# Performance work log

Hardware: AMD Instinct MI355X
Metric: run time of the kernel (lower is better)

## Reference

```python
import jax, jax.numpy as jnp
import numpy as np

N_HEADS = 4
D_HEAD = 64
SCALE = D_HEAD ** -0.5


def setup_inputs() -> dict:
    key = jax.random.key(0)
    k0, k1, k2, k3, k4 = jax.random.split(key, 5)
    C = 256
    return {
        "x": jax.random.normal(k0, (32, C, 32, 32), dtype=jnp.float32),
        "W_qkv": jax.random.normal(k1, (C, 3 * N_HEADS * D_HEAD), dtype=jnp.float32) * 0.02,
        "b_qkv": jax.random.normal(k2, (3 * N_HEADS * D_HEAD,), dtype=jnp.float32) * 0.02,
        "W_out": jax.random.normal(k3, (C, C), dtype=jnp.float32) * 0.02,
        "b_out": jax.random.normal(k4, (C,), dtype=jnp.float32) * 0.02,
    }


def reference(x, W_qkv, b_qkv, W_out, b_out):
    b, c, h, w = x.shape
    # [B, C, H, W] -> [B, S, C], S = H*W  (NOTE: GroupNorm is defined in the
    # original module but never applied in forward; we match that exactly.)
    xs = x.reshape(b, c, h * w).transpose(0, 2, 1)
    qkv = (xs @ W_qkv + b_qkv).reshape(b, -1, N_HEADS, 3 * D_HEAD)
    q, k, v = jnp.split(qkv, 3, axis=-1)  # each [B, S, H, D]
    scores = jnp.einsum('bihd,bjhd->bijh', q, k) * SCALE  # [B, S, S, H]
    attn = jax.nn.softmax(scores, axis=2)  # softmax over key index j
    res = jnp.einsum('bijh,bjhd->bihd', attn, v).reshape(b, -1, N_HEADS * D_HEAD)
    res = res @ W_out + b_out + xs
    return res.transpose(0, 2, 1).reshape(b, c, h, w)
```

## Files before the change

### kernel.cpp

```cpp
#include <hip/hip_runtime.h>

#define NH 4
#define DH 64
#define SS 1024
#define CC 256

typedef __attribute__((ext_vector_type(8))) short short8;
typedef __attribute__((ext_vector_type(4))) float floatx4;
typedef __attribute__((ext_vector_type(16))) float floatx16;
typedef __attribute__((ext_vector_type(2))) unsigned uint2v;

#define MFMA16(a, b, c) __builtin_amdgcn_mfma_f32_16x16x32_bf16(a, b, c, 0, 0, 0)
#define MFMA32(a, b, c) __builtin_amdgcn_mfma_f32_32x32x16_bf16(a, b, c, 0, 0, 0)

#define QSCALE 0.18033688011112042f

__device__ __forceinline__ short f2bf(float f) {
    union { float f; unsigned u; } v; v.f = f;
    unsigned r = (v.u + 0x7fffu + ((v.u >> 16) & 1u)) >> 16;
    return (short)r;
}
__device__ __forceinline__ unsigned bfrn(float f) {
    union { float f; unsigned u; } v; v.f = f;
    return (v.u + 0x7fffu + ((v.u >> 16) & 1u)) >> 16;
}
__device__ __forceinline__ unsigned pk2_trunc(float a, float b) {
    union { float f; unsigned u; } ua, ub; ua.f = a; ub.f = b;
    return (ua.u >> 16) | (ub.u & 0xFFFF0000u);
}
__device__ __forceinline__ unsigned pk2_rn(float a, float b) {
    return bfrn(a) | (bfrn(b) << 16);
}

__global__ __launch_bounds__(256) void k_prep(const float* __restrict__ x,
                                              const float* __restrict__ Wqkv,
                                              const float* __restrict__ Wout,
                                              short* __restrict__ xs,
                                              short* __restrict__ Wqkv_t,
                                              short* __restrict__ Wout_t) {
    int bid = blockIdx.x;
    if (bid < 2048) {
        __shared__ float tile[64][65];
        int b = bid >> 6;
        int s0 = ((bid >> 2) & 15) * 64;
        int c0 = (bid & 3) * 64;
        int t = threadIdx.x;
        int tx = t & 63, ty = t >> 6;
        for (int i = 0; i < 16; ++i) {
            int c = ty + i * 4;
            tile[tx][c] = x[((b * CC) + (c0 + c)) * SS + s0 + tx];
        }
        __syncthreads();
        for (int i = 0; i < 8; ++i) {
            int s = (t >> 5) + i * 8;
            int cp = (t & 31) * 2;
            short2 v;
            v.x = f2bf(tile[s][cp]);
            v.y = f2bf(tile[s][cp + 1]);
            *(short2*)(&xs[((b * SS) + (s0 + s)) * CC + c0 + cp]) = v;
        }
    } else {
        int idx = (bid - 2048) * 256 + threadIdx.x;
        if (idx < 768 * 256) {
            int n = idx >> 8, k = idx & 255;
            Wqkv_t[idx] = f2bf(Wqkv[k * 768 + n]);
        } else {
            int j = idx - 768 * 256;
            int c = j >> 8, k = j & 255;
            Wout_t[j] = f2bf(Wout[k * 256 + c]);
        }
    }
}

__global__ __launch_bounds__(256) void k_qkv(const short* __restrict__ xs,
                                             const short* __restrict__ Wt,
                                             const float* __restrict__ bqkv,
                                             short* __restrict__ qtw,
                                             short* __restrict__ kw,
                                             short* __restrict__ vtw) {
    __shared__ short smem[10240];
    short* As = smem;
    short* Bs = smem + 5120;
    int bid = blockIdx.x;
    int idx = bid >> 3;
    int m0 = ((bid & 7) * 32 + idx / 6) * 128;
    int n0 = (idx % 6) * 128;
    int t = threadIdx.x;
    int lane = t & 63, wid = t >> 6;
    int wr = wid >> 1, wc = wid & 1;
    int c16 = lane & 15, qd = lane >> 4;

    floatx4 acc[4][4] = {};
    short8 pa[2], pb[2];

    for (int j = 0; j < 2; ++j) {
        int id = j * 256 + t, row = id >> 2, cc = id & 3;
        pa[j] = *(const short8*)(&xs[(m0 + row) * CC + cc * 8]);
        pb[j] = *(const short8*)(&Wt[(n0 + row) * CC + cc * 8]);
    }
    for (int kt = 0; kt < 8; ++kt) {
        if (kt) __syncthreads();
        for (int j = 0; j < 2; ++j) {
            int id = j * 256 + t, row = id >> 2, cc = id & 3;
            *(short8*)(&As[row * 40 + cc * 8]) = pa[j];
            *(short8*)(&Bs[row * 40 + cc * 8]) = pb[j];
        }
        __syncthreads();
        if (kt < 7) {
            for (int j = 0; j < 2; ++j) {
                int id = j * 256 + t, row = id >> 2, cc = id & 3;
                pa[j] = *(const short8*)(&xs[(m0 + row) * CC + (kt + 1) * 32 + cc * 8]);
                pb[j] = *(const short8*)(&Wt[(n0 + row) * CC + (kt + 1) * 32 + cc * 8]);
            }
        }
        short8 av[4], bv[4];
        for (int i = 0; i < 4; ++i) {
            av[i] = *(const short8*)(&As[(wr * 64 + i * 16 + c16) * 40 + qd * 8]);
            bv[i] = *(const short8*)(&Bs[(wc * 64 + i * 16 + c16) * 40 + qd * 8]);
        }
        for (int mi = 0; mi < 4; ++mi)
            for (int ni = 0; ni < 4; ++ni)
                acc[mi][ni] = MFMA16(av[mi], bv[ni], acc[mi][ni]);
    }

    int b = m0 >> 10, sbase = m0 & 1023;
    int seg = (n0 >> 6) + wc;
    float bias4[4];
    for (int ni = 0; ni < 4; ++ni)
        bias4[ni] = bqkv[n0 + wc * 64 + ni * 16 + c16];

    int seg0 = n0 >> 6;
    short* Tt = smem;
    for (int s2 = 0; s2 < 2; ++s2) {
        int sg = seg0 + s2;
        int type = sg % 3;
        if (type == 1) continue;
        float sc = (type == 0) ? QSCALE : 1.f;
        __syncthreads();
        if (wc == s2) {
            for (int mi = 0; mi < 4; ++mi)
                for (int ni = 0; ni < 4; ++ni)
                    for (int r = 0; r < 4; ++r)
                        Tt[(ni * 16 + c16) * 136 + wr * 64 + mi * 16 + qd * 4 + r] =
                            f2bf((acc[mi][ni][r] + bias4[ni]) * sc);
        }
        __syncthreads();
        short* dst = ((type == 0) ? qtw : vtw) + (size_t)((b * NH + sg / 3) * DH) * SS + sbase;
        for (int it = 0; it < 4; ++it) {
            int c = it * 256 + t;
            int d = c >> 4, off = (c & 15) * 8;
            *(short8*)(dst + (size_t)d * SS + off) =
                *(const short8*)(&Tt[d * 136 + off]);
        }
    }

    int kseg = (seg0 % 3 == 1) ? seg0 : (((seg0 + 1) % 3 == 1) ? seg0 + 1 : -1);
    if (kseg >= 0) {
        short* Kt = smem;
        __syncthreads();
        if (seg == kseg) {
            for (int mi = 0; mi < 4; ++mi)
                for (int ni = 0; ni < 4; ++ni)
                    for (int r = 0; r < 4; ++r)
                        Kt[(wr * 64 + mi * 16 + qd * 4 + r) * 72 + ni * 16 + c16] =
                            f2bf(acc[mi][ni][r] + bias4[ni]);
        }
        __syncthreads();
        int bhk = b * NH + kseg / 3;
        int srow = t >> 1, dh = (t & 1) * 32;
        short* gdst = &kw[(size_t)(bhk * SS + sbase + srow) * DH + dh];
        const short* lsrc = &Kt[srow * 72 + dh];
        for (int k = 0; k < 4; ++k)
            *(short8*)(gdst + k * 8) = *(const short8*)(lsrc + k * 8);
    }
}

__global__ __launch_bounds__(256) void k_attn(const short* __restrict__ qtw,
                                              const short* __restrict__ kw,
                                              const short* __restrict__ vtw,
                                              short* __restrict__ res) {
    __shared__ __align__(16) short Ks[128 * 72];
    __shared__ __align__(16) short Vts[64 * 136];
    int bid = blockIdx.x;
    int q0 = (bid >> 7) * 128;
    int bh = bid & 127;
    int t = threadIdx.x;
    int lane = t & 63, w = t >> 6;
    int l31 = lane & 31, hi = lane >> 5;
    const short* qp = qtw + (size_t)bh * DH * SS;
    const short* kp = kw + (size_t)bh * SS * DH;
    const short* vp = vtw + (size_t)bh * DH * SS;

    short8 qfrag[4];
    {
        int s = q0 + w * 32 + l31;
        for (int kd = 0; kd < 4; ++kd) {
            short8 q;
            for (int e = 0; e < 8; ++e)
                q[e] = qp[(size_t)(kd * 16 + hi * 8 + e) * SS + s];
            qfrag[kd] = q;
        }
    }

    float l_i = 0.f;
    floatx16 o_acc[2] = {};

    short8 kreg[4], vreg[4];
    for (int j = 0; j < 4; ++j) {
        int L = j * 256 + t;
        int kr = L >> 3, kc = (L & 7) * 8;
        kreg[j] = *(const short8*)(&kp[kr * DH + kc]);
        int vd = L >> 4, vc = (L & 15) * 8;
        vreg[j] = *(const short8*)(&vp[vd * SS + vc]);
    }

    for (int kt = 0; kt < 8; ++kt) {
        if (kt) __syncthreads();
        for (int j = 0; j < 4; ++j) {
            int L = j * 256 + t;
            int kr = L >> 3, kc = (L & 7) * 8;
            *(short8*)(&Ks[kr * 72 + kc]) = kreg[j];
            int vd = L >> 4, vc = (L & 15) * 8;
            *(short8*)(&Vts[vd * 136 + vc]) = vreg[j];
        }
        __syncthreads();
        if (kt < 7) {
            for (int j = 0; j < 4; ++j) {
                int L = j * 256 + t;
                int kr = L >> 3, kc = (L & 7) * 8;
                kreg[j] = *(const short8*)(&kp[((kt + 1) * 128 + kr) * DH + kc]);
                int vd = L >> 4, vc = (L & 15) * 8;
                vreg[j] = *(const short8*)(&vp[vd * SS + (kt + 1) * 128 + vc]);
            }
        }

#pragma unroll
        for (int jt = 0; jt < 4; ++jt) {
            short8 kf[4];
#pragma unroll
            for (int kd = 0; kd < 4; ++kd)
                kf[kd] = *(const short8*)(&Ks[(jt * 32 + l31) * 72 + kd * 16 + hi * 8]);
            short8 vf0[2], vf1[2];
#pragma unroll
            for (int dt = 0; dt < 2; ++dt) {
                vf0[dt] = *(const short8*)(&Vts[(dt * 32 + l31) * 136 + (jt * 2 + 0) * 16 + hi * 8]);
                vf1[dt] = *(const short8*)(&Vts[(dt * 32 + l31) * 136 + (jt * 2 + 1) * 16 + hi * 8]);
            }

            floatx16 sacc = {};
            __builtin_amdgcn_s_setprio(1);
#pragma unroll
            for (int kd = 0; kd < 4; ++kd)
                sacc = MFMA32(kf[kd], qfrag[kd], sacc);
            __builtin_amdgcn_s_setprio(0);

            float ls = 0.f;
            unsigned u[8];
#pragma unroll
            for (int r = 0; r < 16; r += 2) {
                float e0 = __builtin_amdgcn_exp2f(sacc[r]);
                float e1 = __builtin_amdgcn_exp2f(sacc[r + 1]);
                ls += e0 + e1;
                u[r >> 1] = pk2_trunc(e0, e1);
            }
            l_i += ls;

            uint2v r02 = __builtin_amdgcn_permlane32_swap(u[0], u[2], false, false);
            uint2v r13 = __builtin_amdgcn_permlane32_swap(u[1], u[3], false, false);
            uint2v r46 = __builtin_amdgcn_permlane32_swap(u[4], u[6], false, false);
            uint2v r57 = __builtin_amdgcn_permlane32_swap(u[5], u[7], false, false);
            union { unsigned w[4]; short8 s; } pf0, pf1;
            pf0.w[0] = r02[0]; pf0.w[1] = r13[0]; pf0.w[2] = r02[1]; pf0.w[3] = r13[1];
            pf1.w[0] = r46[0]; pf1.w[1] = r57[0]; pf1.w[2] = r46[1]; pf1.w[3] = r57[1];

            __builtin_amdgcn_s_setprio(1);
#pragma unroll
            for (int dt = 0; dt < 2; ++dt) {
                o_acc[dt] = MFMA32(vf0[dt], pf0.s, o_acc[dt]);
                o_acc[dt] = MFMA32(vf1[dt], pf1.s, o_acc[dt]);
            }
            __builtin_amdgcn_s_setprio(0);
        }
    }

    int b = bh >> 2, h = bh & 3;
    {
        float l = l_i;
        l += __shfl_xor(l, 32);
        float inv = 1.f / l;
        int s = q0 + w * 32 + l31;
        long base = (long)(b * SS + s) * CC + h * DH;
#pragma unroll
        for (int dt = 0; dt < 2; ++dt) {
#pragma unroll
            for (int q = 0; q < 4; ++q) {
                int d = dt * 32 + q * 8 + hi * 4;
                uint2 ow;
                ow.x = pk2_rn(o_acc[dt][q * 4 + 0] * inv, o_acc[dt][q * 4 + 1] * inv);
                ow.y = pk2_rn(o_acc[dt][q * 4 + 2] * inv, o_acc[dt][q * 4 + 3] * inv);
                *(uint2*)(&res[base + d]) = ow;
            }
        }
    }
}

__global__ __launch_bounds__(256) void k_out(const short* __restrict__ res,
                                             const short* __restrict__ Wot,
                                             const float* __restrict__ bout,
                                             const float* __restrict__ x,
                                             float* __restrict__ out) {
    __shared__ short As[2][64 * 40];
    __shared__ short Bs[2][128 * 40];
    int b = blockIdx.z;
    int m0 = blockIdx.y * 64;
    int n0 = blockIdx.x * 128;
    int t = threadIdx.x;
    int lane = t & 63, wid = t >> 6;
    int wr = wid >> 1, wc = wid & 1;
    int c16 = lane & 15, qd = lane >> 4;

    floatx4 acc[2][4] = {};
    int arow = t >> 2, ac4 = (t & 3) * 8;
    int brow0 = t >> 2, bc0 = (t & 3) * 8;
    int brow1 = brow0 + 64;
    short8 pa, pb0, pb1;
    pa  = *(const short8*)(&Wot[(m0 + arow) * CC + ac4]);
    pb0 = *(const short8*)(&res[(b * SS + n0 + brow0) * CC + bc0]);
    pb1 = *(const short8*)(&res[(b * SS + n0 + brow1) * CC + bc0]);
    *(short8*)(&As[0][arow * 40 + ac4]) = pa;
    *(short8*)(&Bs[0][brow0 * 40 + bc0]) = pb0;
    *(short8*)(&Bs[0][brow1 * 40 + bc0]) = pb1;
    __syncthreads();

    int cur = 0;
    for (int kt = 0; kt < 8; ++kt) {
        if (kt < 7) {
            pa  = *(const short8*)(&Wot[(m0 + arow) * CC + (kt + 1) * 32 + ac4]);
            pb0 = *(const short8*)(&res[(b * SS + n0 + brow0) * CC + (kt + 1) * 32 + bc0]);
            pb1 = *(const short8*)(&res[(b * SS + n0 + brow1) * CC + (kt + 1) * 32 + bc0]);
        }
        short8 av[2], bv[4];
        for (int i = 0; i < 2; ++i)
            av[i] = *(const short8*)(&As[cur][(wr * 32 + i * 16 + c16) * 40 + qd * 8]);
        for (int i = 0; i < 4; ++i)
            bv[i] = *(const short8*)(&Bs[cur][(wc * 64 + i * 16 + c16) * 40 + qd * 8]);
        for (int mi = 0; mi < 2; ++mi)
            for (int ni = 0; ni < 4; ++ni)
                acc[mi][ni] = MFMA16(av[mi], bv[ni], acc[mi][ni]);
        if (kt < 7) {
            *(short8*)(&As[cur ^ 1][arow * 40 + ac4]) = pa;
            *(short8*)(&Bs[cur ^ 1][brow0 * 40 + bc0]) = pb0;
            *(short8*)(&Bs[cur ^ 1][brow1 * 40 + bc0]) = pb1;
            __syncthreads();
            cur ^= 1;
        }
    }

    for (int mi = 0; mi < 2; ++mi) {
        for (int r = 0; r < 4; ++r) {
            int c = m0 + wr * 32 + mi * 16 + qd * 4 + r;
            float bias = bout[c];
            for (int ni = 0; ni < 4; ++ni) {
                int s = n0 + wc * 64 + ni * 16 + c16;
                float v = acc[mi][ni][r] + bias + x[((b * CC) + c) * SS + s];
                out[((b * CC) + c) * SS + s] = v;
            }
        }
    }
}

extern "C" void kernel_launch(void* const* d_in, const int* in_sizes, int n_in,
                              void* d_out, int out_size, void* d_ws, size_t ws_size,
                              hipStream_t stream) {
    const float* x    = (const float*)d_in[0];
    const float* Wqkv = (const float*)d_in[1];
    const float* bqkv = (const float*)d_in[2];
    const float* Wout = (const float*)d_in[3];
    const float* bout = (const float*)d_in[4];
    float* out = (float*)d_out;

    char* ws = (char*)d_ws;
    short* xs_res = (short*)(ws);
    short* qtw    = (short*)(ws + 16777216);
    short* kw     = (short*)(ws + 33554432);
    short* vtw    = (short*)(ws + 50331648);
    short* Wqkv_t = (short*)(ws + 67108864);
    short* Wout_t = (short*)(ws + 67502080);

    k_prep<<<dim3(3072), 256, 0, stream>>>(x, Wqkv, Wout, xs_res, Wqkv_t, Wout_t);
    k_qkv<<<dim3(1536), 256, 0, stream>>>(xs_res, Wqkv_t, bqkv, qtw, kw, vtw);
    k_attn<<<dim3(1024), 256, 0, stream>>>(qtw, kw, vtw, xs_res);
    k_out<<<dim3(8, 4, 32), 256, 0, stream>>>(xs_res, Wout_t, bout, x, out);
}
```

Before: 179.2 us.

## Use 512-thread attention blocks with 256 queries and 64-key tiles

The attention kernel now runs 8 waves per block, covering 256 query rows each, over half as many blocks. K/V tiles shrink from 128 to 64 keys, giving 16 iterations with one register-prefetched short8 per thread. The goal is more K/V reuse per shared-memory load and less LDS use per block. The trade-off is twice as many barriers per key span and fewer blocks to spread across CUs, which could hurt occupancy or load balance.

```diff
diff --git a/kernel.cpp b/kernel.cpp
--- a/kernel.cpp
+++ b/kernel.cpp
@@ -175,14 +175,14 @@
     }
 }
 
-__global__ __launch_bounds__(256) void k_attn(const short* __restrict__ qtw,
+__global__ __launch_bounds__(512) void k_attn(const short* __restrict__ qtw,
                                               const short* __restrict__ kw,
                                               const short* __restrict__ vtw,
                                               short* __restrict__ res) {
-    __shared__ __align__(16) short Ks[128 * 72];
-    __shared__ __align__(16) short Vts[64 * 136];
+    __shared__ __align__(16) short Ks[64 * 72];
+    __shared__ __align__(16) short Vts[64 * 72];
     int bid = blockIdx.x;
-    int q0 = (bid >> 7) * 128;
+    int q0 = (bid >> 7) * 256;
     int bh = bid & 127;
     int t = threadIdx.x;
     int lane = t & 63, w = t >> 6;
@@ -205,37 +205,23 @@
     float l_i = 0.f;
     floatx16 o_acc[2] = {};
 
-    short8 kreg[4], vreg[4];
-    for (int j = 0; j < 4; ++j) {
-        int L = j * 256 + t;
-        int kr = L >> 3, kc = (L & 7) * 8;
-        kreg[j] = *(const short8*)(&kp[kr * DH + kc]);
-        int vd = L >> 4, vc = (L & 15) * 8;
-        vreg[j] = *(const short8*)(&vp[vd * SS + vc]);
-    }
-
-    for (int kt = 0; kt < 8; ++kt) {
+    int kr = t >> 3, kc = (t & 7) * 8;
+    short8 kreg, vreg;
+    kreg = *(const short8*)(&kp[kr * DH + kc]);
+    vreg = *(const short8*)(&vp[kr * SS + kc]);
+
+    for (int kt = 0; kt < 16; ++kt) {
         if (kt) __syncthreads();
-        for (int j = 0; j < 4; ++j) {
-            int L = j * 256 + t;
-            int kr = L >> 3, kc = (L & 7) * 8;
-            *(short8*)(&Ks[kr * 72 + kc]) = kreg[j];
-            int vd = L >> 4, vc = (L & 15) * 8;
-            *(short8*)(&Vts[vd * 136 + vc]) = vreg[j];
-        }
-        __syncthreads();
-        if (kt < 7) {
-            for (int j = 0; j < 4; ++j) {
-                int L = j * 256 + t;
-                int kr = L >> 3, kc = (L & 7) * 8;
-                kreg[j] = *(const short8*)(&kp[((kt + 1) * 128 + kr) * DH + kc]);
-                int vd = L >> 4, vc = (L & 15) * 8;
-                vreg[j] = *(const short8*)(&vp[vd * SS + (kt + 1) * 128 + vc]);
-            }
-        }
-
-#pragma unroll
-        for (int jt = 0; jt < 4; ++jt) {
+        *(short8*)(&Ks[kr * 72 + kc]) = kreg;
+        *(short8*)(&Vts[kr * 72 + kc]) = vreg;
+        __syncthreads();
+        if (kt < 15) {
+            kreg = *(const short8*)(&kp[((kt + 1) * 64 + kr) * DH + kc]);
+            vreg = *(const short8*)(&vp[kr * SS + (kt + 1) * 64 + kc]);
+        }
+
+#pragma unroll
+        for (int jt = 0; jt < 2; ++jt) {
             short8 kf[4];
 #pragma unroll
             for (int kd = 0; kd < 4; ++kd)
@@ -243,8 +229,8 @@
             short8 vf0[2], vf1[2];
 #pragma unroll
             for (int dt = 0; dt < 2; ++dt) {
-                vf0[dt] = *(const short8*)(&Vts[(dt * 32 + l31) * 136 + (jt * 2 + 0) * 16 + hi * 8]);
-                vf1[dt] = *(const short8*)(&Vts[(dt * 32 + l31) * 136 + (jt * 2 + 1) * 16 + hi * 8]);
+                vf0[dt] = *(const short8*)(&Vts[(dt * 32 + l31) * 72 + (jt * 2 + 0) * 16 + hi * 8]);
+                vf1[dt] = *(const short8*)(&Vts[(dt * 32 + l31) * 72 + (jt * 2 + 1) * 16 + hi * 8]);
             }
 
             floatx16 sacc = {};
@@ -389,6 +375,6 @@
 
     k_prep<<<dim3(3072), 256, 0, stream>>>(x, Wqkv, Wout, xs_res, Wqkv_t, Wout_t);
     k_qkv<<<dim3(1536), 256, 0, stream>>>(xs_res, Wqkv_t, bqkv, qtw, kw, vtw);
-    k_attn<<<dim3(1024), 256, 0, stream>>>(qtw, kw, vtw, xs_res);
+    k_attn<<<dim3(512), 512, 0, stream>>>(qtw, kw, vtw, xs_res);
     k_out<<<dim3(8, 4, 32), 256, 0, stream>>>(xs_res, Wout_t, bout, x, out);
 }
```

After: 171.2 us. 1.05x faster.
